# Kernel optimization log

Hardware: AMD Instinct MI355X
Metric: run time of the kernel (lower is better)

## Reference

```python
import jax, jax.numpy as jnp
import numpy as np

N_NODES = 100000
DIN = 512
B = 1024
T_STEPS = 6
DOUT = 512


def setup_inputs() -> dict:
    key = jax.random.key(0)
    ks = jax.random.split(key, 8)
    s = 0.02  # small init scale for numerical sanity
    x = jax.random.normal(ks[0], (N_NODES, DIN), jnp.float32)
    batch = jnp.sort(jax.random.randint(ks[1], (N_NODES,), 0, B)).astype(jnp.int64)
    Wih = jax.random.normal(ks[2], (4 * DIN, 2 * DIN), jnp.float32) * s
    Whh = jax.random.normal(ks[3], (4 * DIN, DIN), jnp.float32) * s
    bih = jax.random.normal(ks[4], (4 * DIN,), jnp.float32) * s
    bhh = jax.random.normal(ks[5], (4 * DIN,), jnp.float32) * s
    Wpost = jax.random.normal(ks[6], (DOUT, 2 * DIN), jnp.float32) * s
    bpost = jax.random.normal(ks[7], (DOUT,), jnp.float32) * s
    return {"x": x, "batch": batch, "Wih": Wih, "Whh": Whh, "bih": bih,
            "bhh": bhh, "Wpost": Wpost, "bpost": bpost, "num_graphs": B}


def reference(x, batch, Wih, Whh, bih, bhh, Wpost, bpost, num_graphs):
    din = x.shape[1]
    Bg = num_graphs
    h = jnp.zeros((Bg, din), x.dtype)
    c = jnp.zeros((Bg, din), x.dtype)
    q_star = jnp.zeros((Bg, 2 * din), x.dtype)  # [q, r]
    for _ in range(T_STEPS):
        # single-layer LSTM cell over the "batch of graphs" axis
        z = q_star @ Wih.T + h @ Whh.T + (bih + bhh)  # [B, 4*din]
        i, f, g, o = jnp.split(z, 4, axis=-1)  # torch gate order i,f,g,o
        c = jax.nn.sigmoid(f) * c + jax.nn.sigmoid(i) * jnp.tanh(g)
        h = jax.nn.sigmoid(o) * jnp.tanh(c)
        q = h  # [B, din]
        # segment (scatter) softmax attention over nodes of each graph
        e = jnp.sum(x * q[batch], axis=-1)  # [N]
        emax = jax.ops.segment_max(e, batch, num_segments=Bg)
        ex = jnp.exp(e - emax[batch])
        denom = jax.ops.segment_sum(ex, batch, num_segments=Bg)
        a = ex / denom[batch]  # [N]
        r = jax.ops.segment_sum(a[:, None] * x, batch, num_segments=Bg)  # [B, din]
        q_star = jnp.concatenate([q, r], axis=-1)
    # post_pool: Linear(2*din -> dim_out) + bias + ReLU (dropout=0, eval mode)
    out = jax.nn.relu(q_star @ Wpost.T + bpost)
    return out
```

## Files before the change

### kernel.cpp

```cpp
#include <hip/hip_runtime.h>
#include <stdint.h>
#include <stddef.h>

#define DIN    512
#define BGR    1024
#define NGATE  2048
#define KQ     1024
#define DOUT   512
#define TSTEPS 6

typedef unsigned short ushort_t;
typedef short bf16x8 __attribute__((ext_vector_type(8)));
typedef unsigned short u16x8 __attribute__((ext_vector_type(8)));
typedef float f32x4 __attribute__((ext_vector_type(4)));

__device__ __forceinline__ float b2f(unsigned short u) {
    unsigned int i = ((unsigned int)u) << 16;
    float f;
    __builtin_memcpy(&f, &i, 4);
    return f;
}

__device__ __forceinline__ unsigned short f2b(float f) {
    unsigned int i;
    __builtin_memcpy(&i, &f, 4);
    unsigned int lsb = (i >> 16) & 1u;
    i += 0x7fffu + lsb;
    return (unsigned short)(i >> 16);
}

__device__ __forceinline__ float fast_sigmoid(float v) {
    return 1.f / (1.f + __expf(-v));
}

__device__ __forceinline__ float fast_tanh(float v) {
    float t = fabsf(v);
    float e = __expf(-2.f * t);
    float r = (1.f - e) / (1.f + e);
    return v < 0.f ? -r : r;
}

__global__ void probe_dtypes(const ushort_t* x, const ushort_t* Wih,
                             const ushort_t* Whh, const ushort_t* bih,
                             const ushort_t* bhh, const ushort_t* Wpost,
                             const ushort_t* bpost, int* flags)
{
    __shared__ int cnt[7];
    const int tid = threadIdx.x;
    if (tid < 7) cnt[tid] = 0;
    __syncthreads();
    const int t = tid >> 5;
    const int l = tid & 31;
    if (t < 7) {
        const ushort_t* p = (t == 0) ? x : (t == 1) ? Wih : (t == 2) ? Whh
                          : (t == 3) ? bih : (t == 4) ? bhh
                          : (t == 5) ? Wpost : bpost;
        int good = 0;
        for (int i = 0; i < 4; i++) {
            ushort_t u = p[(l * 4 + i) * 2];
            int ex = (u >> 7) & 0xFF;
            if (ex == 0 || (ex >= 96 && ex <= 143)) good++;
        }
        atomicAdd(&cnt[t], good);
    }
    __syncthreads();
    if (tid < 7) flags[tid] = (cnt[tid] < 96) ? 1 : 0;
}

#define BM 64
#define BN 64
#define BK 32

template <int MODE>
__global__ __launch_bounds__(256)
void gemm_bt(const ushort_t* __restrict__ Ag, const ushort_t* __restrict__ Bg,
             const float* __restrict__ bias, float* __restrict__ Cout,
             int M, int N, int K)
{
    __shared__ __align__(16) ushort_t As[BM * BK];
    __shared__ __align__(16) ushort_t Bs[BN * BK];

    const int tid  = threadIdx.x;
    const int lane = tid & 63;
    const int w    = tid >> 6;
    const int wr   = w >> 1;
    const int wc   = w & 1;
    const int lrow = lane & 15;
    const int quad = lane >> 4;

    const int n0 = blockIdx.x * BN;
    const int m0 = blockIdx.y * BM;

    const int srow = tid >> 2;
    const int scol = (tid & 3) * 8;

    f32x4 acc[2][2];
#pragma unroll
    for (int i = 0; i < 2; i++)
#pragma unroll
        for (int j = 0; j < 2; j++)
            acc[i][j] = (f32x4){0.f, 0.f, 0.f, 0.f};

    for (int kt = 0; kt < K; kt += BK) {
        bf16x8 av = *(const bf16x8*)(Ag + ((size_t)(m0 + srow) * K + kt + scol));
        bf16x8 bv = *(const bf16x8*)(Bg + ((size_t)(n0 + srow) * K + kt + scol));
        __syncthreads();
        *(bf16x8*)&As[srow * BK + scol] = av;
        *(bf16x8*)&Bs[srow * BK + scol] = bv;
        __syncthreads();

        bf16x8 af[2], bfr[2];
#pragma unroll
        for (int mi = 0; mi < 2; mi++)
            af[mi] = *(const bf16x8*)&As[(wr * 32 + mi * 16 + lrow) * BK + quad * 8];
#pragma unroll
        for (int ni = 0; ni < 2; ni++)
            bfr[ni] = *(const bf16x8*)&Bs[(wc * 32 + ni * 16 + lrow) * BK + quad * 8];

#pragma unroll
        for (int mi = 0; mi < 2; mi++)
#pragma unroll
            for (int ni = 0; ni < 2; ni++)
                acc[mi][ni] = __builtin_amdgcn_mfma_f32_16x16x32_bf16(
                    af[mi], bfr[ni], acc[mi][ni], 0, 0, 0);
    }

#pragma unroll
    for (int mi = 0; mi < 2; mi++) {
#pragma unroll
        for (int ni = 0; ni < 2; ni++) {
#pragma unroll
            for (int r = 0; r < 4; r++) {
                int gm = m0 + wr * 32 + mi * 16 + quad * 4 + r;
                int gn = n0 + wc * 32 + ni * 16 + lrow;
                float v = acc[mi][ni][r] + bias[gn];
                if (MODE == 1) {
                    if (!(v > 0.f) && (v == v)) v = 0.f;
                }
                Cout[(size_t)gm * N + gn] = v;
            }
        }
    }
}

template <int XMODE>
__global__ __launch_bounds__(256)
void attn_step(const ushort_t* __restrict__ xbsrc, const ushort_t* __restrict__ xraw,
               ushort_t* __restrict__ xbdst, const int* __restrict__ offs,
               const float* __restrict__ z, float* __restrict__ c,
               ushort_t* __restrict__ A, const int* __restrict__ flags)
{
    const int b    = blockIdx.x;
    const int tid  = threadIdx.x;
    const int lane = tid & 63;
    const int w    = tid >> 6;
    const int xf   = (XMODE == 0) ? 0 : flags[0];

    __shared__ float qsh[DIN];
    __shared__ float accL[4][DIN];
    __shared__ float mw[4], lw[4];

    const float* zrow = z + (size_t)b * NGATE;
    for (int d = tid; d < DIN; d += 256) {
        float zi = zrow[d];
        float zf = zrow[DIN + d];
        float zg = zrow[2 * DIN + d];
        float zo = zrow[3 * DIN + d];
        float cc = c[(size_t)b * DIN + d];
        cc = fast_sigmoid(zf) * cc + fast_sigmoid(zi) * fast_tanh(zg);
        float hh = fast_sigmoid(zo) * fast_tanh(cc);
        c[(size_t)b * DIN + d] = cc;
        A[(size_t)b * KQ + d]  = f2b(hh);
        qsh[d] = hh;
    }
    __syncthreads();

    const int s  = offs[b];
    const int en = offs[b + 1];

    float q8[8];
#pragma unroll
    for (int j = 0; j < 8; j++) q8[j] = qsh[lane * 8 + j];

    const float NEG_INF = -__builtin_inff();
    float m = NEG_INF, l = 0.f;
    float acc[8];
#pragma unroll
    for (int j = 0; j < 8; j++) acc[j] = 0.f;

    auto load_row = [&](int n, float* v) {
        if (XMODE == 0 || !xf) {
            const ushort_t* src = (XMODE == 0) ? xbsrc : xraw;
            u16x8 xv = *(const u16x8*)(src + (size_t)n * DIN + lane * 8);
#pragma unroll
            for (int j = 0; j < 8; j++) v[j] = b2f(xv[j]);
            if (XMODE == 1)
                *(u16x8*)(xbdst + (size_t)n * DIN + lane * 8) = xv;
        } else {
            const float* xp = (const float*)xraw;
            f32x4 v0 = *(const f32x4*)(xp + (size_t)n * DIN + lane * 8);
            f32x4 v1 = *(const f32x4*)(xp + (size_t)n * DIN + lane * 8 + 4);
#pragma unroll
            for (int j = 0; j < 4; j++) { v[j] = v0[j]; v[4 + j] = v1[j]; }
            if (XMODE == 1) {
                u16x8 o;
#pragma unroll
                for (int j = 0; j < 8; j++) o[j] = f2b(v[j]);
                *(u16x8*)(xbdst + (size_t)n * DIN + lane * 8) = o;
            }
        }
    };

    auto update = [&](float e, const float* xv) {
        float mn = fmaxf(m, e);
        float al = __expf(m - mn);
        float pp = __expf(e - mn);
        l = l * al + pp;
#pragma unroll
        for (int j = 0; j < 8; j++) acc[j] = acc[j] * al + pp * xv[j];
        m = mn;
    };

    float xa[8] = {0.f}, xc[8] = {0.f};
    int n = s + w;
    if (n < en)     load_row(n, xa);
    if (n + 4 < en) load_row(n + 4, xc);
    for (; n < en; n += 8) {
        float pa[8], pc[8];
        const int np = n + 8;
        if (np < en)     load_row(np, pa);
        if (np + 4 < en) load_row(np + 4, pc);

        float e1 = 0.f, e2 = 0.f;
#pragma unroll
        for (int j = 0; j < 8; j++) { e1 += q8[j] * xa[j]; e2 += q8[j] * xc[j]; }
#pragma unroll
        for (int off = 32; off > 0; off >>= 1) {
            e1 += __shfl_xor(e1, off, 64);
            e2 += __shfl_xor(e2, off, 64);
        }

        update(e1, xa);
        if (n + 4 < en) update(e2, xc);

#pragma unroll
        for (int j = 0; j < 8; j++) { xa[j] = pa[j]; xc[j] = pc[j]; }
    }

    if (lane == 0) { mw[w] = m; lw[w] = l; }
#pragma unroll
    for (int j = 0; j < 8; j++) accL[w][lane * 8 + j] = acc[j];
    __syncthreads();

    const float M = fmaxf(fmaxf(mw[0], mw[1]), fmaxf(mw[2], mw[3]));
    const int d0 = tid * 2;
    float r0 = 0.f, r1 = 0.f, lt = 0.f;
#pragma unroll
    for (int ww = 0; ww < 4; ww++) {
        float mwv = mw[ww];
        float a = (mwv == NEG_INF) ? 0.f : __expf(mwv - M);
        lt += a * lw[ww];
        r0 += a * accL[ww][d0];
        r1 += a * accL[ww][d0 + 1];
    }
    float inv = lt > 0.f ? 1.f / lt : 0.f;
    A[(size_t)b * KQ + DIN + d0]     = f2b(r0 * inv);
    A[(size_t)b * KQ + DIN + d0 + 1] = f2b(r1 * inv);
}

__global__ void prep_weights(const ushort_t* __restrict__ Wih,
                             const ushort_t* __restrict__ Whh,
                             const ushort_t* __restrict__ bih,
                             const ushort_t* __restrict__ bhh,
                             const ushort_t* __restrict__ Wpost,
                             const ushort_t* __restrict__ bpost,
                             ushort_t* __restrict__ Wp,
                             float* __restrict__ biasz,
                             float* __restrict__ biaspost,
                             ushort_t* __restrict__ Wpb,
                             const int* __restrict__ flags)
{
    const int idx = blockIdx.x * 256 + threadIdx.x;
    const int fWih = flags[1], fWhh = flags[2], fbih = flags[3];
    const int fbhh = flags[4], fWpo = flags[5], fbpo = flags[6];

    if (idx < NGATE * KQ) {
        int j = idx >> 10;
        int k = idx & 1023;
        float v = fWih ? ((const float*)Wih)[idx] : b2f(Wih[idx]);
        if (k < DIN) {
            int widx = j * DIN + k;
            v += fWhh ? ((const float*)Whh)[widx] : b2f(Whh[widx]);
        }
        Wp[idx] = f2b(v);
    }
    if (idx < DOUT * KQ) {
        Wpb[idx] = fWpo ? f2b(((const float*)Wpost)[idx]) : Wpost[idx];
    }
    if (idx < NGATE) {
        float v1 = fbih ? ((const float*)bih)[idx] : b2f(bih[idx]);
        float v2 = fbhh ? ((const float*)bhh)[idx] : b2f(bhh[idx]);
        biasz[idx] = v1 + v2;
    }
    if (idx < DOUT) {
        biaspost[idx] = fbpo ? ((const float*)bpost)[idx] : b2f(bpost[idx]);
    }
}

__global__ void prep_state(ushort_t* __restrict__ A, float* __restrict__ c)
{
    int idx = blockIdx.x * 256 + threadIdx.x;
    if (idx < BGR * KQ)  A[idx] = 0;
    if (idx < BGR * DIN) c[idx] = 0.f;
}

__global__ void prep_offsets(const int* __restrict__ batch, int* __restrict__ offs, int Nn)
{
    int n = blockIdx.x * 256 + threadIdx.x;
    if (n >= Nn) return;
    const bool is64 = batch[Nn - 1] < batch[Nn - 2];
    int cur  = is64 ? batch[2 * n] : batch[n];
    int prev = (n == 0) ? -1 : (is64 ? batch[2 * (n - 1)] : batch[n - 1]);
    for (int bb = prev + 1; bb <= cur; ++bb) offs[bb] = n;
    if (n == Nn - 1) {
        for (int bb = cur + 1; bb <= BGR; ++bb) offs[bb] = Nn;
    }
}

extern "C" void kernel_launch(void* const* d_in, const int* in_sizes, int n_in,
                              void* d_out, int out_size, void* d_ws, size_t ws_size,
                              hipStream_t stream)
{
    const ushort_t* x     = (const ushort_t*)d_in[0];
    const int*      batch = (const int*)d_in[1];
    const ushort_t* Wih   = (const ushort_t*)d_in[2];
    const ushort_t* Whh   = (const ushort_t*)d_in[3];
    const ushort_t* bih   = (const ushort_t*)d_in[4];
    const ushort_t* bhh   = (const ushort_t*)d_in[5];
    const ushort_t* Wpost = (const ushort_t*)d_in[6];
    const ushort_t* bpost = (const ushort_t*)d_in[7];
    const int Nn = in_sizes[1];
    const long long Tx = (long long)in_sizes[0];

    char* p = (char*)d_ws;
    auto carve = [&](size_t bytes) -> void* {
        char* q = p;
        p += (bytes + 255) & ~(size_t)255;
        return (void*)q;
    };
    ushort_t* Wp       = (ushort_t*)carve((size_t)NGATE * KQ * 2);
    ushort_t* Wpb      = (ushort_t*)carve((size_t)DOUT * KQ * 2);
    float*    biasz    = (float*)carve((size_t)NGATE * 4);
    float*    biaspost = (float*)carve((size_t)DOUT * 4);
    float*    z        = (float*)carve((size_t)BGR * NGATE * 4);
    float*    c        = (float*)carve((size_t)BGR * DIN * 4);
    ushort_t* A        = (ushort_t*)carve((size_t)BGR * KQ * 2);
    int*      offs     = (int*)carve((size_t)(BGR + 1) * 4);
    int*      flags    = (int*)carve(16 * 4);
    size_t used = (size_t)(p - (char*)d_ws);
    const bool use_xb = (ws_size >= used + (size_t)Tx * 2 + 256);
    ushort_t* xb = use_xb ? (ushort_t*)carve((size_t)Tx * 2) : nullptr;

    probe_dtypes<<<1, 256, 0, stream>>>(x, Wih, Whh, bih, bhh, Wpost, bpost, flags);
    prep_weights<<<(NGATE * KQ) / 256, 256, 0, stream>>>(
        Wih, Whh, bih, bhh, Wpost, bpost, Wp, biasz, biaspost, Wpb, flags);
    prep_state<<<(BGR * KQ) / 256, 256, 0, stream>>>(A, c);
    prep_offsets<<<(Nn + 255) / 256, 256, 0, stream>>>(batch, offs, Nn);

    for (int t = 0; t < TSTEPS; ++t) {
        gemm_bt<0><<<dim3(NGATE / BN, BGR / BM), 256, 0, stream>>>(
            A, Wp, biasz, z, BGR, NGATE, KQ);
        if (use_xb) {
            if (t == 0)
                attn_step<1><<<BGR, 256, 0, stream>>>(xb, x, xb, offs, z, c, A, flags);
            else
                attn_step<0><<<BGR, 256, 0, stream>>>(xb, x, xb, offs, z, c, A, flags);
        } else {
            attn_step<2><<<BGR, 256, 0, stream>>>(x, x, nullptr, offs, z, c, A, flags);
        }
    }
    gemm_bt<1><<<dim3(DOUT / BN, BGR / BM), 256, 0, stream>>>(
        A, Wpb, biaspost, (float*)d_out, BGR, DOUT, KQ);
}
```

Measured before the change: 569.6 us.

## Fuse LSTM cell into gate GEMM epilogue via interleaved weight layout

Reorders the combined gate weights so each 64-column GEMM tile holds matching i,f,g,o slices for 16 hidden units. The LSTM cell update then runs in the GEMM epilogue, writing c and h directly instead of a full fp32 z matrix that attn_step had to re-read. The first step's GEMM is skipped because the initial state is zero, so h0 and c0 come from the biases alone in a new prep kernel. It also adds register prefetch of the next K tile in both GEMMs. Each gemm_cell block now does 4 MFMAs per wave per K step, which may change occupancy and latency hiding.

```diff
diff --git a/kernel.cpp b/kernel.cpp
--- a/kernel.cpp
+++ b/kernel.cpp
@@ -71,6 +71,79 @@
 #define BN 64
 #define BK 32
 
+__global__ __launch_bounds__(256)
+void gemm_cell(const ushort_t* __restrict__ Ag,
+               const ushort_t* __restrict__ Wg,
+               const float* __restrict__ bias2,
+               float* __restrict__ c, float* __restrict__ H)
+{
+    __shared__ __align__(16) ushort_t As[BM * BK];
+    __shared__ __align__(16) ushort_t Bs[BM * BK];
+
+    const int tid  = threadIdx.x;
+    const int lane = tid & 63;
+    const int w    = tid >> 6;
+    const int lrow = lane & 15;
+    const int quad = lane >> 4;
+
+    const int n0 = blockIdx.x * 64;
+    const int m0 = blockIdx.y * BM;
+
+    const int srow = tid >> 2;
+    const int scol = (tid & 3) * 8;
+
+    const ushort_t* aSrc = Ag + (size_t)(m0 + srow) * KQ + scol;
+    const ushort_t* bSrc = Wg + (size_t)(n0 + srow) * KQ + scol;
+
+    f32x4 acc[4];
+#pragma unroll
+    for (int ni = 0; ni < 4; ni++) acc[ni] = (f32x4){0.f, 0.f, 0.f, 0.f};
+
+    bf16x8 av = *(const bf16x8*)(aSrc);
+    bf16x8 bv = *(const bf16x8*)(bSrc);
+
+    for (int kt = 0; kt < KQ; kt += BK) {
+        __syncthreads();
+        *(bf16x8*)&As[srow * BK + scol] = av;
+        *(bf16x8*)&Bs[srow * BK + scol] = bv;
+        if (kt + BK < KQ) {
+            av = *(const bf16x8*)(aSrc + kt + BK);
+            bv = *(const bf16x8*)(bSrc + kt + BK);
+        }
+        __syncthreads();
+
+        bf16x8 af = *(const bf16x8*)&As[(w * 16 + lrow) * BK + quad * 8];
+        bf16x8 bfr[4];
+#pragma unroll
+        for (int ni = 0; ni < 4; ni++)
+            bfr[ni] = *(const bf16x8*)&Bs[(ni * 16 + lrow) * BK + quad * 8];
+#pragma unroll
+        for (int ni = 0; ni < 4; ni++)
+            acc[ni] = __builtin_amdgcn_mfma_f32_16x16x32_bf16(
+                af, bfr[ni], acc[ni], 0, 0, 0);
+    }
+
+    const int d   = blockIdx.x * 16 + lrow;
+    const float bi = bias2[n0 + lrow];
+    const float bf = bias2[n0 + 16 + lrow];
+    const float bg = bias2[n0 + 32 + lrow];
+    const float bo = bias2[n0 + 48 + lrow];
+#pragma unroll
+    for (int r = 0; r < 4; r++) {
+        const int gm = m0 + w * 16 + quad * 4 + r;
+        float zi = acc[0][r] + bi;
+        float zf = acc[1][r] + bf;
+        float zg = acc[2][r] + bg;
+        float zo = acc[3][r] + bo;
+        size_t off = (size_t)gm * DIN + d;
+        float cc = c[off];
+        cc = fast_sigmoid(zf) * cc + fast_sigmoid(zi) * fast_tanh(zg);
+        float hh = fast_sigmoid(zo) * fast_tanh(cc);
+        c[off] = cc;
+        H[off] = hh;
+    }
+}
+
 template <int MODE>
 __global__ __launch_bounds__(256)
 void gemm_bt(const ushort_t* __restrict__ Ag, const ushort_t* __restrict__ Bg,
@@ -94,6 +167,9 @@
     const int srow = tid >> 2;
     const int scol = (tid & 3) * 8;
 
+    const ushort_t* aSrc = Ag + (size_t)(m0 + srow) * K + scol;
+    const ushort_t* bSrc = Bg + (size_t)(n0 + srow) * K + scol;
+
     f32x4 acc[2][2];
 #pragma unroll
     for (int i = 0; i < 2; i++)
@@ -101,12 +177,17 @@
         for (int j = 0; j < 2; j++)
             acc[i][j] = (f32x4){0.f, 0.f, 0.f, 0.f};
 
+    bf16x8 av = *(const bf16x8*)(aSrc);
+    bf16x8 bv = *(const bf16x8*)(bSrc);
+
     for (int kt = 0; kt < K; kt += BK) {
-        bf16x8 av = *(const bf16x8*)(Ag + ((size_t)(m0 + srow) * K + kt + scol));
-        bf16x8 bv = *(const bf16x8*)(Bg + ((size_t)(n0 + srow) * K + kt + scol));
         __syncthreads();
         *(bf16x8*)&As[srow * BK + scol] = av;
         *(bf16x8*)&Bs[srow * BK + scol] = bv;
+        if (kt + BK < K) {
+            av = *(const bf16x8*)(aSrc + kt + BK);
+            bv = *(const bf16x8*)(bSrc + kt + BK);
+        }
         __syncthreads();
 
         bf16x8 af[2], bfr[2];
@@ -147,8 +228,8 @@
 __global__ __launch_bounds__(256)
 void attn_step(const ushort_t* __restrict__ xbsrc, const ushort_t* __restrict__ xraw,
                ushort_t* __restrict__ xbdst, const int* __restrict__ offs,
-               const float* __restrict__ z, float* __restrict__ c,
-               ushort_t* __restrict__ A, const int* __restrict__ flags)
+               const float* __restrict__ H, ushort_t* __restrict__ A,
+               const int* __restrict__ flags)
 {
     const int b    = blockIdx.x;
     const int tid  = threadIdx.x;
@@ -156,31 +237,21 @@
     const int w    = tid >> 6;
     const int xf   = (XMODE == 0) ? 0 : flags[0];
 
-    __shared__ float qsh[DIN];
     __shared__ float accL[4][DIN];
     __shared__ float mw[4], lw[4];
 
-    const float* zrow = z + (size_t)b * NGATE;
-    for (int d = tid; d < DIN; d += 256) {
-        float zi = zrow[d];
-        float zf = zrow[DIN + d];
-        float zg = zrow[2 * DIN + d];
-        float zo = zrow[3 * DIN + d];
-        float cc = c[(size_t)b * DIN + d];
-        cc = fast_sigmoid(zf) * cc + fast_sigmoid(zi) * fast_tanh(zg);
-        float hh = fast_sigmoid(zo) * fast_tanh(cc);
-        c[(size_t)b * DIN + d] = cc;
-        A[(size_t)b * KQ + d]  = f2b(hh);
-        qsh[d] = hh;
-    }
-    __syncthreads();
+    const float* hrow = H + (size_t)b * DIN;
+    {
+        const int d0 = tid * 2;
+        A[(size_t)b * KQ + d0]     = f2b(hrow[d0]);
+        A[(size_t)b * KQ + d0 + 1] = f2b(hrow[d0 + 1]);
+    }
+    f32x4 q0 = *(const f32x4*)(hrow + lane * 8);
+    f32x4 q1 = *(const f32x4*)(hrow + lane * 8 + 4);
+    float q8[8] = {q0[0], q0[1], q0[2], q0[3], q1[0], q1[1], q1[2], q1[3]};
 
     const int s  = offs[b];
     const int en = offs[b + 1];
-
-    float q8[8];
-#pragma unroll
-    for (int j = 0; j < 8; j++) q8[j] = qsh[lane * 8 + j];
 
     const float NEG_INF = -__builtin_inff();
     float m = NEG_INF, l = 0.f;
@@ -275,7 +346,7 @@
                              const ushort_t* __restrict__ Wpost,
                              const ushort_t* __restrict__ bpost,
                              ushort_t* __restrict__ Wp,
-                             float* __restrict__ biasz,
+                             float* __restrict__ bias2,
                              float* __restrict__ biaspost,
                              ushort_t* __restrict__ Wpb,
                              const int* __restrict__ flags)
@@ -285,12 +356,15 @@
     const int fbhh = flags[4], fWpo = flags[5], fbpo = flags[6];
 
     if (idx < NGATE * KQ) {
-        int j = idx >> 10;
-        int k = idx & 1023;
-        float v = fWih ? ((const float*)Wih)[idx] : b2f(Wih[idx]);
+        const int nn = idx >> 10;
+        const int k  = idx & 1023;
+        const int g  = (nn >> 4) & 3;
+        const int n  = g * 512 + (nn >> 6) * 16 + (nn & 15);
+        const int widx = n * KQ + k;
+        float v = fWih ? ((const float*)Wih)[widx] : b2f(Wih[widx]);
         if (k < DIN) {
-            int widx = j * DIN + k;
-            v += fWhh ? ((const float*)Whh)[widx] : b2f(Whh[widx]);
+            int hidx = n * DIN + k;
+            v += fWhh ? ((const float*)Whh)[hidx] : b2f(Whh[hidx]);
         }
         Wp[idx] = f2b(v);
     }
@@ -298,20 +372,41 @@
         Wpb[idx] = fWpo ? f2b(((const float*)Wpost)[idx]) : Wpost[idx];
     }
     if (idx < NGATE) {
-        float v1 = fbih ? ((const float*)bih)[idx] : b2f(bih[idx]);
-        float v2 = fbhh ? ((const float*)bhh)[idx] : b2f(bhh[idx]);
-        biasz[idx] = v1 + v2;
+        const int g = (idx >> 4) & 3;
+        const int n = g * 512 + (idx >> 6) * 16 + (idx & 15);
+        float v1 = fbih ? ((const float*)bih)[n] : b2f(bih[n]);
+        float v2 = fbhh ? ((const float*)bhh)[n] : b2f(bhh[n]);
+        bias2[idx] = v1 + v2;
     }
     if (idx < DOUT) {
         biaspost[idx] = fbpo ? ((const float*)bpost)[idx] : b2f(bpost[idx]);
     }
 }
 
-__global__ void prep_state(ushort_t* __restrict__ A, float* __restrict__ c)
-{
-    int idx = blockIdx.x * 256 + threadIdx.x;
-    if (idx < BGR * KQ)  A[idx] = 0;
-    if (idx < BGR * DIN) c[idx] = 0.f;
+__global__ void prep_h0(const ushort_t* __restrict__ bih,
+                        const ushort_t* __restrict__ bhh,
+                        float* __restrict__ c, float* __restrict__ H,
+                        ushort_t* __restrict__ A, const int* __restrict__ flags)
+{
+    const int b   = blockIdx.x;
+    const int tid = threadIdx.x;
+    const int fbih = flags[3], fbhh = flags[4];
+    for (int d = tid; d < DIN; d += 256) {
+        auto ld = [&](int n) {
+            float v1 = fbih ? ((const float*)bih)[n] : b2f(bih[n]);
+            float v2 = fbhh ? ((const float*)bhh)[n] : b2f(bhh[n]);
+            return v1 + v2;
+        };
+        float zi = ld(d);
+        float zg = ld(2 * DIN + d);
+        float zo = ld(3 * DIN + d);
+        float c0 = fast_sigmoid(zi) * fast_tanh(zg);
+        float h0 = fast_sigmoid(zo) * fast_tanh(c0);
+        c[(size_t)b * DIN + d] = c0;
+        H[(size_t)b * DIN + d] = h0;
+        A[(size_t)b * KQ + d]       = f2b(h0);
+        A[(size_t)b * KQ + DIN + d] = 0;
+    }
 }
 
 __global__ void prep_offsets(const int* __restrict__ batch, int* __restrict__ offs, int Nn)
@@ -350,10 +445,10 @@
     };
     ushort_t* Wp       = (ushort_t*)carve((size_t)NGATE * KQ * 2);
     ushort_t* Wpb      = (ushort_t*)carve((size_t)DOUT * KQ * 2);
-    float*    biasz    = (float*)carve((size_t)NGATE * 4);
+    float*    bias2    = (float*)carve((size_t)NGATE * 4);
     float*    biaspost = (float*)carve((size_t)DOUT * 4);
-    float*    z        = (float*)carve((size_t)BGR * NGATE * 4);
     float*    c        = (float*)carve((size_t)BGR * DIN * 4);
+    float*    H        = (float*)carve((size_t)BGR * DIN * 4);
     ushort_t* A        = (ushort_t*)carve((size_t)BGR * KQ * 2);
     int*      offs     = (int*)carve((size_t)(BGR + 1) * 4);
     int*      flags    = (int*)carve(16 * 4);
@@ -363,20 +458,21 @@
 
     probe_dtypes<<<1, 256, 0, stream>>>(x, Wih, Whh, bih, bhh, Wpost, bpost, flags);
     prep_weights<<<(NGATE * KQ) / 256, 256, 0, stream>>>(
-        Wih, Whh, bih, bhh, Wpost, bpost, Wp, biasz, biaspost, Wpb, flags);
-    prep_state<<<(BGR * KQ) / 256, 256, 0, stream>>>(A, c);
+        Wih, Whh, bih, bhh, Wpost, bpost, Wp, bias2, biaspost, Wpb, flags);
+    prep_h0<<<BGR, 256, 0, stream>>>(bih, bhh, c, H, A, flags);
     prep_offsets<<<(Nn + 255) / 256, 256, 0, stream>>>(batch, offs, Nn);
 
     for (int t = 0; t < TSTEPS; ++t) {
-        gemm_bt<0><<<dim3(NGATE / BN, BGR / BM), 256, 0, stream>>>(
-            A, Wp, biasz, z, BGR, NGATE, KQ);
+        if (t > 0)
+            gemm_cell<<<dim3(NGATE / 64, BGR / BM), 256, 0, stream>>>(
+                A, Wp, bias2, c, H);
         if (use_xb) {
             if (t == 0)
-                attn_step<1><<<BGR, 256, 0, stream>>>(xb, x, xb, offs, z, c, A, flags);
+                attn_step<1><<<BGR, 256, 0, stream>>>(xb, x, xb, offs, H, A, flags);
             else
-                attn_step<0><<<BGR, 256, 0, stream>>>(xb, x, xb, offs, z, c, A, flags);
+                attn_step<0><<<BGR, 256, 0, stream>>>(xb, x, xb, offs, H, A, flags);
         } else {
-            attn_step<2><<<BGR, 256, 0, stream>>>(x, x, nullptr, offs, z, c, A, flags);
+            attn_step<2><<<BGR, 256, 0, stream>>>(x, x, nullptr, offs, H, A, flags);
         }
     }
     gemm_bt<1><<<dim3(DOUT / BN, BGR / BM), 256, 0, stream>>>(
```

New measurement: 529.3 us. 7.1% less time.
